# Kernel optimization log

Hardware: AMD Instinct MI355X
Metric: run time of the kernel (lower is better)

Reference implementation:

```python
import jax, jax.numpy as jnp
import numpy as np

N = 10000        # nodes
E = 30000        # edges
NODE_DIM = 16
EDGE_DIM = 8
H = 64           # hidden_dim
L = 3            # n_layers
BNECK = 16       # max(H // 4, 8)
EPS = 1e-5       # BatchNorm eps


def setup_inputs() -> dict:
    key = jax.random.key(0)
    ks = jax.random.split(key, 16)

    def w(k, shape, fan_in):
        return (jax.random.normal(k, shape, dtype=jnp.float32) / np.sqrt(fan_in)).astype(jnp.float32)

    inp = {
        "x": jax.random.normal(ks[0], (N, NODE_DIM), dtype=jnp.float32),
        "edge_index": jax.random.randint(ks[1], (2, E), 0, N, dtype=jnp.int32),
        "edge_attr": jax.random.normal(ks[2], (E, EDGE_DIM), dtype=jnp.float32),
        # input MLP
        "w_in": w(ks[3], (NODE_DIM, H), NODE_DIM),
        "b_in": jnp.zeros((H,), jnp.float32),
        # per-layer edge MLP: edge_dim -> bneck -> H*H
        "ew1": w(ks[4], (L, EDGE_DIM, BNECK), EDGE_DIM),
        "eb1": jnp.zeros((L, BNECK), jnp.float32),
        "ew2": w(ks[5], (L, BNECK, H * H), BNECK),
        "eb2": jnp.zeros((L, H * H), jnp.float32),
        # per-layer NNConv root weight + bias
        "w_root": w(ks[6], (L, H, H), H),
        "conv_bias": jnp.zeros((L, H), jnp.float32),
        # per-layer BatchNorm affine params
        "bn_gamma": jnp.ones((L, H), jnp.float32),
        "bn_beta": jnp.zeros((L, H), jnp.float32),
    }
    return inp


def reference(x, edge_index, edge_attr, w_in, b_in, ew1, eb1, ew2, eb2,
              w_root, conv_bias, bn_gamma, bn_beta):
    src, dst = edge_index[0], edge_index[1]
    # in-degree for mean aggregation (nodes with 0 edges stay 0, matching PyG)
    deg = jax.ops.segment_sum(jnp.ones((E,), jnp.float32), dst, num_segments=N)
    inv_deg = jnp.where(deg > 0, 1.0 / jnp.maximum(deg, 1.0), 0.0)[:, None]  # [N,1]

    # input MLP (dropout = identity in eval)
    h = jax.nn.relu(x @ w_in + b_in)  # [N,H]

    for l in range(L):
        res = h
        # edge MLP -> per-edge weight matrix [E, H, H]
        we = jax.nn.relu(edge_attr @ ew1[l] + eb1[l]) @ ew2[l] + eb2[l]
        we = we.reshape(E, H, H)
        # gather source features, per-edge matmul, scatter-mean to targets
        msg = jnp.einsum('ei,eio->eo', h[src], we)          # [E,H]
        agg = jax.ops.segment_sum(msg, dst, num_segments=N) * inv_deg  # [N,H]
        out = agg + h @ w_root[l] + conv_bias[l]
        # BatchNorm over nodes (batch statistics, biased variance)
        mu = out.mean(axis=0)
        var = out.var(axis=0)
        out = bn_gamma[l] * (out - mu) * jax.lax.rsqrt(var + EPS) + bn_beta[l]
        # ReLU + (dropout identity) + residual
        h = jax.nn.relu(out) + res
    return h
```

## Files before the change

### kernel.cpp

```cpp
#include <hip/hip_runtime.h>
#include <hip/hip_bf16.h>

#define N_NODES 10000
#define N_EDGES 30000
#define ND 16
#define ED 8
#define H 64
#define BNECK 16
#define NLAYERS 3
#define EPSN 1e-5f

#define NCHUNK 17
#define WF_PER_LAYER (NCHUNK * 4096)
#define WFR_PER_LAYER 4096

#define R_WFG (NLAYERS * WF_PER_LAYER)
#define R_WFR (R_WFG + NLAYERS * WFR_PER_LAYER)
#define R_DEG (R_WFR + N_EDGES)
#define R_IN  (R_DEG + N_NODES * H)

typedef __attribute__((ext_vector_type(8))) short short8;
typedef __attribute__((ext_vector_type(4))) float f32x4;

static __device__ __forceinline__ short f2bf(float f) {
    __hip_bfloat16 b = __float2bfloat16(f);
    return __builtin_bit_cast(short, b);
}

__global__ void k_prep(const float* __restrict__ x, const int* __restrict__ dst,
                       const float* __restrict__ w_in, const float* __restrict__ b_in,
                       const float* __restrict__ ew2, const float* __restrict__ eb2,
                       const float* __restrict__ wroot,
                       ushort* __restrict__ wfg, ushort* __restrict__ wfr,
                       float* __restrict__ deg, float* __restrict__ h) {
    int idx = blockIdx.x * 256 + threadIdx.x;
    if (idx < R_WFG) {
        int l = idx / WF_PER_LAYER;
        int r = idx % WF_PER_LAYER;
        int c = r >> 12;
        int q = r & 4095;
        int j    = q & 7;
        int lane = (q >> 3) & 63;
        int ct   = (q >> 9) & 3;
        int s    = q >> 11;
        int k = c * 64 + s * 32 + ((lane >> 4) * 8) + j;
        int o = ct * 16 + (lane & 15);
        float v;
        if (k < 1024) v = ew2[l * 65536 + k * 64 + o];
        else          v = eb2[l * 4096 + (k - 1024) * 64 + o];
        wfg[idx] = __builtin_bit_cast(ushort, __float2bfloat16(v));
    } else if (idx < R_WFR) {
        int r2 = idx - R_WFG;
        int l = r2 / WFR_PER_LAYER;
        int q = r2 % WFR_PER_LAYER;
        int j    = q & 7;
        int lane = (q >> 3) & 63;
        int ct   = (q >> 9) & 3;
        int s    = (q >> 11) & 1;
        int k = s * 32 + ((lane >> 4) * 8) + j;
        int o = ct * 16 + (lane & 15);
        wfr[r2] = __builtin_bit_cast(ushort, __float2bfloat16(wroot[l * 4096 + k * 64 + o]));
    } else if (idx < R_DEG) {
        int e = idx - R_WFR;
        atomicAdd(&deg[dst[e]], 1.0f);
    } else if (idx < R_IN) {
        int i2 = idx - R_DEG;
        int n = i2 >> 6, o = i2 & 63;
        float s = b_in[o];
        #pragma unroll
        for (int d = 0; d < ND; ++d) s += x[n * ND + d] * w_in[d * H + o];
        h[i2] = fmaxf(s, 0.f);
    }
}

__global__ __launch_bounds__(256) void k_msg(
    const float* __restrict__ h, const int* __restrict__ src, const int* __restrict__ dst,
    const float* __restrict__ ea, const float* __restrict__ ew1, const float* __restrict__ eb1,
    const ushort* __restrict__ wf, float* __restrict__ agg)
{
    __shared__ float h_lds[32 * 64];
    __shared__ float t_lds[32][NCHUNK];
    __shared__ float s_agg[32][68];
    __shared__ int s_src[32], s_dst[32];

    const int tid = threadIdx.x;
    const int ebase = blockIdx.x * 32;

    for (int i = tid; i < 32 * 68; i += 256) ((float*)s_agg)[i] = 0.f;
    if (tid < 32) {
        int e = ebase + tid;
        bool v = e < N_EDGES;
        s_src[tid] = src[v ? e : 0];
        s_dst[tid] = v ? dst[e] : -1;
    }
    __syncthreads();

    #pragma unroll
    for (int p = 0; p < 2; ++p) {
        int el = p * 16 + (tid >> 4);
        int c4 = tid & 15;
        f32x4 v = *(const f32x4*)&h[s_src[el] * H + c4 * 4];
        *(f32x4*)&h_lds[el * 64 + ((c4 ^ (el & 15)) << 2)] = v;
    }
    {
        int el = tid >> 3, bg = (tid & 7) * 2;
        int eg = min(ebase + el, N_EDGES - 1);
        float av[8];
        *(f32x4*)&av[0] = *(const f32x4*)&ea[eg * ED];
        *(f32x4*)&av[4] = *(const f32x4*)&ea[eg * ED + 4];
        #pragma unroll
        for (int bb = 0; bb < 2; ++bb) {
            int b = bg + bb;
            float s = eb1[b];
            #pragma unroll
            for (int d = 0; d < ED; ++d) s += av[d] * ew1[d * BNECK + b];
            t_lds[el][b] = fmaxf(s, 0.f);
        }
    }
    if (tid < 32) t_lds[tid][16] = 1.0f;
    __syncthreads();

    const int lane = tid & 63;
    const int w = tid >> 6;
    const int l15 = lane & 15;
    const int lk2 = (lane >> 4) * 2;
    const int er0 = l15;
    const int er1 = l15 + 16;

    f32x4 acc[2][4];
    #pragma unroll
    for (int i = 0; i < 2; ++i)
        #pragma unroll
        for (int j = 0; j < 4; ++j) acc[i][j] = (f32x4){0.f, 0.f, 0.f, 0.f};

#define CHUNK_BODY(cc) do { \
        const int c_ = (cc); \
        const float t0 = t_lds[er0][c_]; \
        const float t1 = t_lds[er1][c_]; \
        _Pragma("unroll") \
        for (int s = 0; s < 2; ++s) { \
            const int c40 = s * 8 + lk2; \
            short8 a0, a1; \
            { \
                const f32x4 xx = *(const f32x4*)&h_lds[er0 * 64 + ((c40 ^ l15) << 2)]; \
                const f32x4 yy = *(const f32x4*)&h_lds[er0 * 64 + (((c40 + 1) ^ l15) << 2)]; \
                a0[0] = f2bf(xx[0] * t0); a0[1] = f2bf(xx[1] * t0); \
                a0[2] = f2bf(xx[2] * t0); a0[3] = f2bf(xx[3] * t0); \
                a0[4] = f2bf(yy[0] * t0); a0[5] = f2bf(yy[1] * t0); \
                a0[6] = f2bf(yy[2] * t0); a0[7] = f2bf(yy[3] * t0); \
            } \
            { \
                const f32x4 xx = *(const f32x4*)&h_lds[er1 * 64 + ((c40 ^ l15) << 2)]; \
                const f32x4 yy = *(const f32x4*)&h_lds[er1 * 64 + (((c40 + 1) ^ l15) << 2)]; \
                a1[0] = f2bf(xx[0] * t1); a1[1] = f2bf(xx[1] * t1); \
                a1[2] = f2bf(xx[2] * t1); a1[3] = f2bf(xx[3] * t1); \
                a1[4] = f2bf(yy[0] * t1); a1[5] = f2bf(yy[1] * t1); \
                a1[6] = f2bf(yy[2] * t1); a1[7] = f2bf(yy[3] * t1); \
            } \
            const ushort* bp = wf + (size_t)(((c_ * 2 + s) * 4) * 64 + lane) * 8; \
            _Pragma("unroll") \
            for (int ct = 0; ct < 4; ++ct) { \
                short8 bfrag = *(const short8*)(bp + ct * 512); \
                acc[0][ct] = __builtin_amdgcn_mfma_f32_16x16x32_bf16(a0, bfrag, acc[0][ct], 0, 0, 0); \
                acc[1][ct] = __builtin_amdgcn_mfma_f32_16x16x32_bf16(a1, bfrag, acc[1][ct], 0, 0, 0); \
            } \
        } \
    } while (0)

    #pragma unroll
    for (int q = 0; q < 4; ++q) { CHUNK_BODY(w * 4 + q); }
    if (w == 3) { CHUNK_BODY(16); }
#undef CHUNK_BODY

    #pragma unroll
    for (int st = 0; st < 2; ++st) {
        #pragma unroll
        for (int r = 0; r < 4; ++r) {
            int row = st * 16 + (lane >> 4) * 4 + r;
            #pragma unroll
            for (int ct = 0; ct < 4; ++ct)
                atomicAdd(&s_agg[row][ct * 16 + l15], acc[st][ct][r]);
        }
    }
    __syncthreads();

    #pragma unroll
    for (int rep = 0; rep < 8; ++rep) {
        int i2 = rep * 256 + tid;
        int row = i2 >> 6, col = i2 & 63;
        int d = s_dst[row];
        if (d >= 0) atomicAdd(&agg[d * H + col], s_agg[row][col]);
    }
}

__global__ __launch_bounds__(64) void k_node1(
    const float* __restrict__ agg, const float* __restrict__ deg, const float* __restrict__ h,
    const ushort* __restrict__ wfr, const float* __restrict__ cb,
    float* __restrict__ out, float* __restrict__ sums)
{
    const int lane = threadIdx.x;
    const int l15 = lane & 15;
    const int lk8 = (lane >> 4) * 8;
    const int nb = blockIdx.x * 16;

    short8 a[2];
    #pragma unroll
    for (int s = 0; s < 2; ++s) {
        const float* hp = &h[(nb + l15) * H + s * 32 + lk8];
        f32x4 xx = *(const f32x4*)hp;
        f32x4 yy = *(const f32x4*)(hp + 4);
        a[s][0] = f2bf(xx[0]); a[s][1] = f2bf(xx[1]); a[s][2] = f2bf(xx[2]); a[s][3] = f2bf(xx[3]);
        a[s][4] = f2bf(yy[0]); a[s][5] = f2bf(yy[1]); a[s][6] = f2bf(yy[2]); a[s][7] = f2bf(yy[3]);
    }
    f32x4 acc[4] = {};
    #pragma unroll
    for (int s = 0; s < 2; ++s)
        #pragma unroll
        for (int ct = 0; ct < 4; ++ct) {
            short8 bfrag = *(const short8*)(wfr + (size_t)(((s * 4 + ct) * 64) + lane) * 8);
            acc[ct] = __builtin_amdgcn_mfma_f32_16x16x32_bf16(a[s], bfrag, acc[ct], 0, 0, 0);
        }

    float ls[4] = {}, lq[4] = {};
    #pragma unroll
    for (int r = 0; r < 4; ++r) {
        int node = nb + (lane >> 4) * 4 + r;
        float dg = deg[node];
        float inv = dg > 0.f ? 1.f / dg : 0.f;
        #pragma unroll
        for (int ct = 0; ct < 4; ++ct) {
            int c = ct * 16 + l15;
            float v = acc[ct][r] + cb[c] + inv * agg[node * H + c];
            out[node * H + c] = v;
            ls[ct] += v;
            lq[ct] += v * v;
        }
    }
    #pragma unroll
    for (int ct = 0; ct < 4; ++ct) {
        ls[ct] += __shfl_xor(ls[ct], 16, 64); ls[ct] += __shfl_xor(ls[ct], 32, 64);
        lq[ct] += __shfl_xor(lq[ct], 16, 64); lq[ct] += __shfl_xor(lq[ct], 32, 64);
    }
    if (lane < 16) {
        #pragma unroll
        for (int ct = 0; ct < 4; ++ct) {
            atomicAdd(&sums[ct * 16 + lane], ls[ct]);
            atomicAdd(&sums[64 + ct * 16 + lane], lq[ct]);
        }
    }
}

__global__ void k_node2(const float* __restrict__ out, const float* __restrict__ sums,
                        const float* __restrict__ gamma, const float* __restrict__ beta,
                        const float* __restrict__ hin, float* __restrict__ hout)
{
    int i4 = blockIdx.x * 256 + threadIdx.x;
    if (i4 >= N_NODES * 16) return;
    f32x4 ob = ((const f32x4*)out)[i4];
    f32x4 hb = ((const f32x4*)hin)[i4];
    int o = (i4 * 4) & 63;
    const float invN = 1.0f / (float)N_NODES;
    f32x4 res;
    #pragma unroll
    for (int j = 0; j < 4; ++j) {
        float mu = sums[o + j] * invN;
        float var = sums[64 + o + j] * invN - mu * mu;
        float scale = gamma[o + j] * rsqrtf(var + EPSN);
        float v = (ob[j] - mu) * scale + beta[o + j];
        res[j] = fmaxf(v, 0.f) + hb[j];
    }
    ((f32x4*)hout)[i4] = res;
}

extern "C" void kernel_launch(void* const* d_in, const int* in_sizes, int n_in,
                              void* d_out, int out_size, void* d_ws, size_t ws_size,
                              hipStream_t stream) {
    const float* x     = (const float*)d_in[0];
    const int*   ei    = (const int*)  d_in[1];
    const float* ea    = (const float*)d_in[2];
    const float* w_in  = (const float*)d_in[3];
    const float* b_in  = (const float*)d_in[4];
    const float* ew1   = (const float*)d_in[5];
    const float* eb1   = (const float*)d_in[6];
    const float* ew2   = (const float*)d_in[7];
    const float* eb2   = (const float*)d_in[8];
    const float* wroot = (const float*)d_in[9];
    const float* cb    = (const float*)d_in[10];
    const float* gamma = (const float*)d_in[11];
    const float* beta  = (const float*)d_in[12];
    float* outp = (float*)d_out;

    float* ws   = (float*)d_ws;
    float* deg  = ws;
    float* agg  = deg + N_NODES;
    float* sums = agg + 3 * N_NODES * H;
    float* h    = sums + 3 * 128;
    float* outb = h + N_NODES * H;
    ushort* wfg = (ushort*)(outb + N_NODES * H);
    ushort* wfr = wfg + NLAYERS * WF_PER_LAYER;

    const int* srcp = ei;
    const int* dstp = ei + N_EDGES;

    hipMemsetAsync(ws, 0, (size_t)(N_NODES + 3 * N_NODES * H + 3 * 128) * sizeof(float), stream);
    k_prep<<<(R_IN + 255) / 256, 256, 0, stream>>>(x, dstp, w_in, b_in, ew2, eb2, wroot,
                                                   wfg, wfr, deg, h);

    for (int l = 0; l < NLAYERS; ++l) {
        float* agg_l  = agg + (size_t)l * N_NODES * H;
        float* sums_l = sums + l * 128;
        k_msg<<<(N_EDGES + 31) / 32, 256, 0, stream>>>(
            h, srcp, dstp, ea,
            ew1 + l * ED * BNECK, eb1 + l * BNECK,
            wfg + (size_t)l * WF_PER_LAYER, agg_l);
        k_node1<<<N_NODES / 16, 64, 0, stream>>>(
            agg_l, deg, h, wfr + (size_t)l * WFR_PER_LAYER, cb + l * H, outb, sums_l);
        float* hout = (l == NLAYERS - 1) ? outp : h;
        k_node2<<<(N_NODES * 16 + 255) / 256, 256, 0, stream>>>(
            outb, sums_l, gamma + l * H, beta + l * H, h, hout);
    }
}
```

Before: 306.1 us.

## Replace atomic scatter aggregation with CSR gather of per-edge messages

Builds a dst-sorted CSR (integer degree count, single-block scan, atomic cursor fill) once per call. k_msg now writes per-edge messages densely, and k_node1 gathers and sums each node's incoming messages through the CSR. This removes global float atomics into agg and the large memset of three agg buffers. In exchange it adds two small launches, including a serial one-block scan, a 30000x64 message buffer write/read, and irregular gathers in k_node1. Summation order also becomes nondeterministic, because the CSR order depends on the atomic cursor.

```diff
diff --git a/kernel.cpp b/kernel.cpp
--- a/kernel.cpp
+++ b/kernel.cpp
@@ -32,7 +32,7 @@
                        const float* __restrict__ ew2, const float* __restrict__ eb2,
                        const float* __restrict__ wroot,
                        ushort* __restrict__ wfg, ushort* __restrict__ wfr,
-                       float* __restrict__ deg, float* __restrict__ h) {
+                       int* __restrict__ deg, float* __restrict__ h) {
     int idx = blockIdx.x * 256 + threadIdx.x;
     if (idx < R_WFG) {
         int l = idx / WF_PER_LAYER;
@@ -62,7 +62,7 @@
         wfr[r2] = __builtin_bit_cast(ushort, __float2bfloat16(wroot[l * 4096 + k * 64 + o]));
     } else if (idx < R_DEG) {
         int e = idx - R_WFR;
-        atomicAdd(&deg[dst[e]], 1.0f);
+        atomicAdd(&deg[dst[e]], 1);
     } else if (idx < R_IN) {
         int i2 = idx - R_DEG;
         int n = i2 >> 6, o = i2 & 63;
@@ -73,15 +73,61 @@
     }
 }
 
+#define PER_T 40
+__global__ __launch_bounds__(256) void k_scan(const int* __restrict__ deg,
+                                              int* __restrict__ offs,
+                                              int* __restrict__ cursor) {
+    __shared__ int lds[256];
+    const int tid = threadIdx.x;
+    const int beg = tid * PER_T;
+    int cnt[PER_T];
+    int s = 0;
+    #pragma unroll
+    for (int i = 0; i < PER_T; ++i) {
+        int n = beg + i;
+        cnt[i] = (n < N_NODES) ? deg[n] : 0;
+        s += cnt[i];
+    }
+    lds[tid] = s;
+    __syncthreads();
+    #pragma unroll
+    for (int off = 1; off < 256; off <<= 1) {
+        int v = (tid >= off) ? lds[tid - off] : 0;
+        __syncthreads();
+        lds[tid] += v;
+        __syncthreads();
+    }
+    int run = lds[tid] - s;
+    #pragma unroll
+    for (int i = 0; i < PER_T; ++i) {
+        int n = beg + i;
+        if (n < N_NODES) {
+            offs[n] = run;
+            cursor[n] = run;
+            run += cnt[i];
+        }
+    }
+    if (tid == 255) offs[N_NODES] = run;
+}
+
+__global__ void k_csr(const int* __restrict__ dst, int* __restrict__ cursor,
+                      int* __restrict__ csr) {
+    int e = blockIdx.x * 256 + threadIdx.x;
+    if (e < N_EDGES) {
+        int p = atomicAdd(&cursor[dst[e]], 1);
+        csr[p] = e;
+    }
+}
+
 __global__ __launch_bounds__(256) void k_msg(
-    const float* __restrict__ h, const int* __restrict__ src, const int* __restrict__ dst,
+    const float* __restrict__ h, const int* __restrict__ src,
     const float* __restrict__ ea, const float* __restrict__ ew1, const float* __restrict__ eb1,
-    const ushort* __restrict__ wf, float* __restrict__ agg)
+    const ushort* __restrict__ wf, float* __restrict__ msg)
 {
     __shared__ float h_lds[32 * 64];
     __shared__ float t_lds[32][NCHUNK];
     __shared__ float s_agg[32][68];
-    __shared__ int s_src[32], s_dst[32];
+    __shared__ int s_src[32];
 
     const int tid = threadIdx.x;
     const int ebase = blockIdx.x * 32;
@@ -89,9 +135,7 @@
     for (int i = tid; i < 32 * 68; i += 256) ((float*)s_agg)[i] = 0.f;
     if (tid < 32) {
         int e = ebase + tid;
-        bool v = e < N_EDGES;
-        s_src[tid] = src[v ? e : 0];
-        s_dst[tid] = v ? dst[e] : -1;
+        s_src[tid] = src[(e < N_EDGES) ? e : 0];
     }
     __syncthreads();
 
@@ -188,14 +232,14 @@
     for (int rep = 0; rep < 8; ++rep) {
         int i2 = rep * 256 + tid;
         int row = i2 >> 6, col = i2 & 63;
-        int d = s_dst[row];
-        if (d >= 0) atomicAdd(&agg[d * H + col], s_agg[row][col]);
+        int e = ebase + row;
+        if (e < N_EDGES) msg[(size_t)e * H + col] = s_agg[row][col];
     }
 }
 
 __global__ __launch_bounds__(64) void k_node1(
-    const float* __restrict__ agg, const float* __restrict__ deg, const float* __restrict__ h,
-    const ushort* __restrict__ wfr, const float* __restrict__ cb,
+    const float* __restrict__ msg, const int* __restrict__ offs, const int* __restrict__ csr,
+    const float* __restrict__ h, const ushort* __restrict__ wfr, const float* __restrict__ cb,
     float* __restrict__ out, float* __restrict__ sums)
 {
     const int lane = threadIdx.x;
@@ -225,12 +269,21 @@
     #pragma unroll
     for (int r = 0; r < 4; ++r) {
         int node = nb + (lane >> 4) * 4 + r;
-        float dg = deg[node];
-        float inv = dg > 0.f ? 1.f / dg : 0.f;
+        int b0 = offs[node], b1 = offs[node + 1];
+        float inv = (b1 > b0) ? 1.f / (float)(b1 - b0) : 0.f;
+        float g0 = 0.f, g1 = 0.f, g2 = 0.f, g3 = 0.f;
+        for (int p = b0; p < b1; ++p) {
+            const float* mr = msg + (size_t)csr[p] * H;
+            g0 += mr[l15];
+            g1 += mr[16 + l15];
+            g2 += mr[32 + l15];
+            g3 += mr[48 + l15];
+        }
+        float gg[4] = {g0, g1, g2, g3};
         #pragma unroll
         for (int ct = 0; ct < 4; ++ct) {
             int c = ct * 16 + l15;
-            float v = acc[ct][r] + cb[c] + inv * agg[node * H + c];
+            float v = acc[ct][r] + cb[c] + inv * gg[ct];
             out[node * H + c] = v;
             ls[ct] += v;
             lq[ct] += v * v;
@@ -290,31 +343,34 @@
     const float* beta  = (const float*)d_in[12];
     float* outp = (float*)d_out;
 
-    float* ws   = (float*)d_ws;
-    float* deg  = ws;
-    float* agg  = deg + N_NODES;
-    float* sums = agg + 3 * N_NODES * H;
-    float* h    = sums + 3 * 128;
-    float* outb = h + N_NODES * H;
-    ushort* wfg = (ushort*)(outb + N_NODES * H);
-    ushort* wfr = wfg + NLAYERS * WF_PER_LAYER;
+    int*    deg    = (int*)d_ws;
+    float*  sums   = (float*)(deg + N_NODES);
+    float*  h      = sums + 3 * 128;
+    float*  outb   = h + N_NODES * H;
+    float*  msg    = outb + N_NODES * H;
+    ushort* wfg    = (ushort*)(msg + (size_t)N_EDGES * H);
+    ushort* wfr    = wfg + NLAYERS * WF_PER_LAYER;
+    int*    offs   = (int*)(wfr + NLAYERS * WFR_PER_LAYER);
+    int*    cursor = offs + N_NODES + 1;
+    int*    csr    = cursor + N_NODES;
 
     const int* srcp = ei;
     const int* dstp = ei + N_EDGES;
 
-    hipMemsetAsync(ws, 0, (size_t)(N_NODES + 3 * N_NODES * H + 3 * 128) * sizeof(float), stream);
+    hipMemsetAsync(d_ws, 0, (size_t)(N_NODES + 3 * 128) * sizeof(int), stream);
     k_prep<<<(R_IN + 255) / 256, 256, 0, stream>>>(x, dstp, w_in, b_in, ew2, eb2, wroot,
                                                    wfg, wfr, deg, h);
+    k_scan<<<1, 256, 0, stream>>>(deg, offs, cursor);
+    k_csr<<<(N_EDGES + 255) / 256, 256, 0, stream>>>(dstp, cursor, csr);
 
     for (int l = 0; l < NLAYERS; ++l) {
-        float* agg_l  = agg + (size_t)l * N_NODES * H;
         float* sums_l = sums + l * 128;
         k_msg<<<(N_EDGES + 31) / 32, 256, 0, stream>>>(
-            h, srcp, dstp, ea,
+            h, srcp, ea,
             ew1 + l * ED * BNECK, eb1 + l * BNECK,
-            wfg + (size_t)l * WF_PER_LAYER, agg_l);
+            wfg + (size_t)l * WF_PER_LAYER, msg);
         k_node1<<<N_NODES / 16, 64, 0, stream>>>(
-            agg_l, deg, h, wfr + (size_t)l * WFR_PER_LAYER, cb + l * H, outb, sums_l);
+            msg, offs, csr, h, wfr + (size_t)l * WFR_PER_LAYER, cb + l * H, outb, sums_l);
         float* hout = (l == NLAYERS - 1) ? outp : h;
         k_node2<<<(N_NODES * 16 + 255) / 256, 256, 0, stream>>>(
             outb, sums_l, gamma + l * H, beta + l * H, h, hout);
```

Measured after the change: 353.8 us. 15.6% more time.
